# Kernel optimization log

Hardware: AMD Instinct MI355X
Metric: run time of the kernel (lower is better)

The kernel has to match this reference:

```python
import jax, jax.numpy as jnp
import numpy as np

B, S, D, H = 2, 4096, 768, 12
DK = D // H


def setup_inputs() -> dict:
    key = jax.random.key(0)
    ks = jax.random.split(key, 12)
    inp = {
        "q": jax.random.normal(ks[0], (B, S, D), dtype=jnp.float32),
        "k": jax.random.normal(ks[1], (B, S, D), dtype=jnp.float32),
        "v": jax.random.normal(ks[2], (B, S, D), dtype=jnp.float32),
        "mask": jax.random.randint(ks[3], (B, 1, 1, S), 0, 2, dtype=jnp.int32),
        "w_q": jax.random.normal(ks[4], (D, D), dtype=jnp.float32) * 0.02,
        "b_q": jnp.zeros((D,), dtype=jnp.float32),
        "w_k": jax.random.normal(ks[5], (D, D), dtype=jnp.float32) * 0.02,
        "b_k": jnp.zeros((D,), dtype=jnp.float32),
        "w_v": jax.random.normal(ks[6], (D, D), dtype=jnp.float32) * 0.02,
        "b_v": jnp.zeros((D,), dtype=jnp.float32),
        "w_o": jax.random.normal(ks[7], (D, D), dtype=jnp.float32) * 0.02,
        "b_o": jnp.zeros((D,), dtype=jnp.float32),
    }
    return inp


def reference(q, k, v, mask, w_q, b_q, w_k, b_k, w_v, b_v, w_o, b_o):
    scale = 1.0 / jnp.sqrt(jnp.asarray(DK, dtype=q.dtype))
    # projections, then split heads: [B, S, H, DK]
    Q = (q @ w_q + b_q).reshape(B, S, H, DK)
    K = (k @ w_k + b_k).reshape(B, S, H, DK)
    V = (v @ w_v + b_v).reshape(B, S, H, DK)
    # scores: [B, H, Sq, Sk]
    scores = jnp.einsum("bqhd,bkhd->bhqk", Q, K) * scale
    scores = jnp.where(mask == 0, jnp.asarray(-1e9, dtype=scores.dtype), scores)
    attn = jax.nn.softmax(scores, axis=-1)
    # dropout prob is 0.0 (eval): identity
    out = jnp.einsum("bhqk,bkhd->bqhd", attn, V).reshape(B, S, D)
    return out @ w_o + b_o
```

## Files before the change

### kernel.cpp

```cpp
#include <hip/hip_runtime.h>
#include <hip/hip_bf16.h>
#include <stdint.h>

typedef __bf16 bf16;
typedef bf16 bf16x8 __attribute__((ext_vector_type(8)));
typedef float f32x4 __attribute__((ext_vector_type(4)));

constexpr int CB  = 2;
constexpr int CS  = 4096;
constexpr int CD  = 768;
constexpr int CH  = 12;
constexpr int CDK = 64;
constexpr int CBH = CB * CH;
constexpr int CM  = CB * CS;

__device__ __forceinline__ void gload16(const void* g, void* l) {
  __builtin_amdgcn_global_load_lds((const __attribute__((address_space(1))) void*)g,
                                   (__attribute__((address_space(3))) void*)l, 16, 0, 0);
}

__device__ __forceinline__ float fast_exp2(float x) {
#if __has_builtin(__builtin_amdgcn_exp2f)
  return __builtin_amdgcn_exp2f(x);
#else
  return exp2f(x);
#endif
}

__device__ __forceinline__ uint32_t cvtpk_bf16(float lo, float hi) {
  uint32_t r;
  asm("v_cvt_pk_bf16_f32 %0, %1, %2" : "=v"(r) : "v"(lo), "v"(hi));
  return r;
}

__global__ __launch_bounds__(256) void k_convert(const float* __restrict__ in,
                                                 bf16* __restrict__ out, int n8) {
  int i = blockIdx.x * 256 + threadIdx.x;
  if (i >= n8) return;
  const float4* p = (const float4*)in;
  float4 a = p[i * 2], b = p[i * 2 + 1];
  bf16x8 o;
  o[0] = (bf16)a.x; o[1] = (bf16)a.y; o[2] = (bf16)a.z; o[3] = (bf16)a.w;
  o[4] = (bf16)b.x; o[5] = (bf16)b.y; o[6] = (bf16)b.z; o[7] = (bf16)b.w;
  ((bf16x8*)out)[i] = o;
}

__global__ __launch_bounds__(256) void k_wtrans(const float* __restrict__ w0, const float* __restrict__ w1,
                                                const float* __restrict__ w2, const float* __restrict__ w3,
                                                bf16* __restrict__ o0, bf16* __restrict__ o1,
                                                bf16* __restrict__ o2, bf16* __restrict__ o3) {
  const float* w; bf16* o;
  if      (blockIdx.z == 0) { w = w0; o = o0; }
  else if (blockIdx.z == 1) { w = w1; o = o1; }
  else if (blockIdx.z == 2) { w = w2; o = o2; }
  else                      { w = w3; o = o3; }
  __shared__ float t[32][33];
  int k0 = blockIdx.x * 32, n0 = blockIdx.y * 32;
  int tx = threadIdx.x & 31, ty = threadIdx.x >> 5;
#pragma unroll
  for (int i = 0; i < 4; ++i) {
    int kk = ty + i * 8;
    t[kk][tx] = w[(size_t)(k0 + kk) * CD + n0 + tx];
  }
  __syncthreads();
#pragma unroll
  for (int i = 0; i < 4; ++i) {
    int nn = ty + i * 8;
    o[(size_t)(n0 + nn) * CD + k0 + tx] = (bf16)t[tx][nn];
  }
}

template <int EPI>
__device__ __forceinline__ void gemm_core(const bf16* __restrict__ A, const bf16* __restrict__ Bt,
                                          const float* __restrict__ bias, void* __restrict__ outp,
                                          int K, int mtile, int ntile) {
  __shared__ bf16 As[2][128 * 32];
  __shared__ bf16 Bs[2][128 * 32];
  const int tid = threadIdx.x;
  const int lane = tid & 63;
  const int wid = tid >> 6;
  const int wr = wid >> 1, wc = wid & 1;
  const int r = lane & 15, g = lane >> 4;
  const int m0 = mtile * 128, n0 = ntile * 128;

  f32x4 acc[4][4] = {};

  auto stageAB = [&](int bsel, int kt) {
#pragma unroll
    for (int i = 0; i < 2; ++i) {
      int flat = tid * 8 + i * 2048;
      int rr = flat >> 5, cc = flat & 31;
      gload16(A + (size_t)(m0 + rr) * K + kt + cc, (char*)&As[bsel][0] + (size_t)flat * 2);
    }
#pragma unroll
    for (int i = 0; i < 2; ++i) {
      int flat = tid * 8 + i * 2048;
      int rr = flat >> 5, cc = flat & 31;
      gload16(Bt + (size_t)(n0 + rr) * K + kt + cc, (char*)&Bs[bsel][0] + (size_t)flat * 2);
    }
  };

  stageAB(0, 0);
  const int NKT = K / 32;
  for (int t = 0; t < NKT; ++t) {
    __syncthreads();
    if (t + 1 < NKT) stageAB((t + 1) & 1, (t + 1) * 32);
    const bf16* Asb = &As[t & 1][0];
    const bf16* Bsb = &Bs[t & 1][0];

    bf16x8 af[4], bfr[4];
#pragma unroll
    for (int mi = 0; mi < 4; ++mi)
      af[mi] = *(const bf16x8*)(Asb + (wr * 64 + mi * 16 + r) * 32 + g * 8);
#pragma unroll
    for (int ni = 0; ni < 4; ++ni)
      bfr[ni] = *(const bf16x8*)(Bsb + (wc * 64 + ni * 16 + r) * 32 + g * 8);
#pragma unroll
    for (int mi = 0; mi < 4; ++mi)
#pragma unroll
      for (int ni = 0; ni < 4; ++ni)
        acc[mi][ni] = __builtin_amdgcn_mfma_f32_16x16x32_bf16(af[mi], bfr[ni], acc[mi][ni], 0, 0, 0);
  }

  if (EPI == 0) {
    bf16* o = (bf16*)outp;
#pragma unroll
    for (int ni = 0; ni < 4; ++ni) {
      int col = n0 + wc * 64 + ni * 16 + r;
      float bv = bias[col];
      int h = col >> 6, dk = col & 63;
#pragma unroll
      for (int mi = 0; mi < 4; ++mi) {
#pragma unroll
        for (int q = 0; q < 4; ++q) {
          int row = m0 + wr * 64 + mi * 16 + g * 4 + q;
          int b = row >> 12, s = row & 4095;
          o[(size_t)((b * CH + h) * CS + s) * CDK + dk] = (bf16)(acc[mi][ni][q] + bv);
        }
      }
    }
  } else {
    float* o = (float*)outp;
#pragma unroll
    for (int ni = 0; ni < 4; ++ni) {
      int col = n0 + wc * 64 + ni * 16 + r;
      float bv = bias[col];
#pragma unroll
      for (int mi = 0; mi < 4; ++mi) {
#pragma unroll
        for (int q = 0; q < 4; ++q) {
          int row = m0 + wr * 64 + mi * 16 + g * 4 + q;
          o[(size_t)row * CD + col] = acc[mi][ni][q] + bv;
        }
      }
    }
  }
}

__global__ __launch_bounds__(256) void k_qkv(const bf16* __restrict__ qb, const bf16* __restrict__ kb,
                                             const bf16* __restrict__ vb,
                                             const bf16* __restrict__ wqT, const bf16* __restrict__ wkT,
                                             const bf16* __restrict__ wvT,
                                             const float* __restrict__ bq, const float* __restrict__ bk,
                                             const float* __restrict__ bv,
                                             bf16* __restrict__ Qh, bf16* __restrict__ Kh,
                                             bf16* __restrict__ Vh) {
  const bf16* A; const bf16* W; const float* bias; bf16* O;
  if      (blockIdx.z == 0) { A = qb; W = wqT; bias = bq; O = Qh; }
  else if (blockIdx.z == 1) { A = kb; W = wkT; bias = bk; O = Kh; }
  else                      { A = vb; W = wvT; bias = bv; O = Vh; }
  gemm_core<0>(A, W, bias, O, CD, blockIdx.x, blockIdx.y);
}

__global__ __launch_bounds__(256) void k_out(const bf16* __restrict__ ao, const bf16* __restrict__ woT,
                                             const float* __restrict__ bo, float* __restrict__ out) {
  gemm_core<1>(ao, woT, bo, out, CD, blockIdx.x, blockIdx.y);
}

__global__ __launch_bounds__(256) void k_scan(const int* __restrict__ mask, int* __restrict__ idx,
                                              int* __restrict__ nk) {
  int b = blockIdx.x;
  const int* m = mask + b * CS;
  int tid = threadIdx.x, lane = tid & 63, wv = tid >> 6;
  int base = tid * 16;
  int mv[16];
  const int4* m4 = (const int4*)(m + base);
#pragma unroll
  for (int i = 0; i < 4; ++i) {
    int4 x = m4[i];
    mv[i * 4 + 0] = x.x; mv[i * 4 + 1] = x.y; mv[i * 4 + 2] = x.z; mv[i * 4 + 3] = x.w;
  }
  int local = 0;
#pragma unroll
  for (int j = 0; j < 16; ++j) local += (mv[j] != 0);
  int pre = local;
#pragma unroll
  for (int d = 1; d < 64; d <<= 1) {
    int t = __shfl_up(pre, d, 64);
    if (lane >= d) pre += t;
  }
  __shared__ int wsum[4];
  if (lane == 63) wsum[wv] = pre;
  __syncthreads();
  int woff = 0;
  for (int w = 0; w < wv; ++w) woff += wsum[w];
  int pos = woff + pre - local;
  int* ib = idx + b * CS;
#pragma unroll
  for (int j = 0; j < 16; ++j)
    if (mv[j]) ib[pos++] = base + j;
  if (tid == 255) nk[b] = woff + pre;
}

__global__ __launch_bounds__(256) void k_gather(const bf16* __restrict__ Kh, const bf16* __restrict__ Vh,
                                                const int* __restrict__ idx, const int* __restrict__ nk,
                                                bf16* __restrict__ Kc, bf16* __restrict__ VTc) {
  int bh = blockIdx.y, b = bh / CH;
  int nkb = nk[b];
  int nkp = (nkb + 63) & ~63;
  int i0 = blockIdx.x * 64;
  if (i0 >= nkp) return;
  const int* ib = idx + b * CS;
  int tid = threadIdx.x;
  __shared__ bf16 t[64][72];
#pragma unroll
  for (int i = 0; i < 2; ++i) {
    int f = tid + i * 256;
    int ii = f >> 3, c8 = (f & 7) << 3;
    int gi = i0 + ii;
    bf16x8 kv = {}, vv = {};
    if (gi < nkb) {
      int s = ib[gi];
      kv = *(const bf16x8*)&Kh[((size_t)bh * CS + s) * CDK + c8];
      vv = *(const bf16x8*)&Vh[((size_t)bh * CS + s) * CDK + c8];
    }
    *(bf16x8*)&Kc[((size_t)bh * CS + gi) * CDK + c8] = kv;
#pragma unroll
    for (int j = 0; j < 8; ++j) t[ii][c8 + j] = vv[j];
  }
  __syncthreads();
#pragma unroll
  for (int i = 0; i < 2; ++i) {
    int f = tid + i * 256;
    int d = f >> 3, s8 = (f & 7) << 3;
    bf16x8 vv;
#pragma unroll
    for (int j = 0; j < 8; ++j) vv[j] = t[s8 + j][d];
    *(bf16x8*)&VTc[((size_t)bh * CDK + d) * CS + i0 + s8] = vv;
  }
}

__global__ __launch_bounds__(256) void k_attn(const bf16* __restrict__ Qh, const bf16* __restrict__ Kc,
                                              const bf16* __restrict__ VTc, const int* __restrict__ nk,
                                              bf16* __restrict__ attn_out) {
  __shared__ bf16 Ks[2][64 * 64];
  __shared__ bf16 VTs[2][64 * 64];
  __shared__ bf16 Pl[4][16 * 64];

  const int tid = threadIdx.x;
  const int lane = tid & 63, wv = tid >> 6;
  const int r = lane & 15, g = lane >> 4;
  const int bh = blockIdx.y;
  const int b = bh / CH, h = bh % CH;
  const int q0 = blockIdx.x * 128 + wv * 32;
  const int nkb = nk[b];
  const int ntiles = (nkb + 63) >> 6;

  bf16x8 aq[2][2];
#pragma unroll
  for (int rg = 0; rg < 2; ++rg) {
    size_t qrow = (size_t)bh * CS + q0 + rg * 16 + r;
    aq[rg][0] = *(const bf16x8*)&Qh[qrow * CDK + g * 8];
    aq[rg][1] = *(const bf16x8*)&Qh[qrow * CDK + 32 + g * 8];
  }

  f32x4 accO[2][4] = {};
  float m_run[2] = {0.f, 0.f}, l_run[2] = {0.f, 0.f};

  const float cs = 0.18033688f;
  char* PlB = (char*)&Pl[wv][0];

  auto stage = [&](int bsel, int kt) {
    char* KsB0 = (char*)&Ks[bsel][0];
    char* VTsB0 = (char*)&VTs[bsel][0];
#pragma unroll
    for (int i = 0; i < 2; ++i) {
      int f = tid + i * 256;
      int row = f >> 3, sl = f & 7;
      int srcb = (sl * 16) ^ ((row & 7) << 4);
      gload16(Kc + (size_t)(bh * CS + kt + row) * CDK + (srcb >> 1), KsB0 + (size_t)f * 16);
    }
#pragma unroll
    for (int i = 0; i < 2; ++i) {
      int f = tid + i * 256;
      int row = f >> 3, sl = f & 7;
      int srcb = (sl * 16) ^ ((row & 7) << 4);
      gload16(VTc + (size_t)(bh * CDK + row) * CS + kt + (srcb >> 1), VTsB0 + (size_t)f * 16);
    }
  };

  stage(0, 0);

  for (int t = 0; t < ntiles; ++t) {
    __syncthreads();
    if (t + 1 < ntiles) stage((t + 1) & 1, (t + 1) * 64);
    const int kt = t * 64;
    char* KsB = (char*)&Ks[t & 1][0];
    char* VTsB = (char*)&VTs[t & 1][0];
    const bool tail = (kt + 64 > nkb);

#pragma unroll
    for (int rg = 0; rg < 2; ++rg) {
      float p[16];
#pragma unroll
      for (int kb = 0; kb < 4; ++kb) {
        f32x4 s = {};
#pragma unroll
        for (int kh = 0; kh < 2; ++kh) {
          int key = kb * 16 + r;
          int byteoff = key * 128 + ((kh * 64 + g * 16) ^ ((key & 7) << 4));
          bf16x8 ka = *(const bf16x8*)(KsB + byteoff);
          s = __builtin_amdgcn_mfma_f32_16x16x32_bf16(ka, aq[rg][kh], s, 0, 0, 0);
        }
#pragma unroll
        for (int q = 0; q < 4; ++q) p[kb * 4 + q] = s[q] * cs;
      }
      if (tail) {
#pragma unroll
        for (int kb = 0; kb < 4; ++kb)
#pragma unroll
          for (int q = 0; q < 4; ++q)
            if (kt + kb * 16 + g * 4 + q >= nkb) p[kb * 4 + q] = -1e30f;
      }

      float pm = p[0];
#pragma unroll
      for (int j = 1; j < 16; ++j) pm = fmaxf(pm, p[j]);
      pm = fmaxf(pm, __shfl_xor(pm, 16, 64));
      pm = fmaxf(pm, __shfl_xor(pm, 32, 64));

      if (__any(pm > m_run[rg] + 8.f)) {
        float mnew = fmaxf(m_run[rg], pm);
        float corr = fast_exp2(m_run[rg] - mnew);
        m_run[rg] = mnew;
        l_run[rg] *= corr;
#pragma unroll
        for (int q = 0; q < 4; ++q) {
          float cq = __shfl(corr, 20 * g + q, 64);
#pragma unroll
          for (int nb = 0; nb < 4; ++nb) accO[rg][nb][q] *= cq;
        }
      }

      float rsum = 0.f;
#pragma unroll
      for (int kb = 0; kb < 4; ++kb) {
        float e0 = fast_exp2(p[kb * 4 + 0] - m_run[rg]);
        float e1 = fast_exp2(p[kb * 4 + 1] - m_run[rg]);
        float e2 = fast_exp2(p[kb * 4 + 2] - m_run[rg]);
        float e3 = fast_exp2(p[kb * 4 + 3] - m_run[rg]);
        rsum += (e0 + e1) + (e2 + e3);
        uint2 w;
        w.x = cvtpk_bf16(e0, e1);
        w.y = cvtpk_bf16(e2, e3);
        int byteoff = r * 128 + ((kb * 32 + g * 8) ^ ((r & 7) << 4));
        *(uint2*)(PlB + byteoff) = w;
      }
      rsum += __shfl_xor(rsum, 16, 64);
      rsum += __shfl_xor(rsum, 32, 64);
      l_run[rg] += rsum;

      bf16x8 pa[2];
#pragma unroll
      for (int kh = 0; kh < 2; ++kh) {
        int byteoff = r * 128 + ((kh * 64 + g * 16) ^ ((r & 7) << 4));
        pa[kh] = *(const bf16x8*)(PlB + byteoff);
      }
#pragma unroll
      for (int nb = 0; nb < 4; ++nb) {
#pragma unroll
        for (int kh = 0; kh < 2; ++kh) {
          int d = nb * 16 + r;
          int byteoff = d * 128 + ((kh * 64 + g * 16) ^ ((d & 7) << 4));
          bf16x8 bvf = *(const bf16x8*)(VTsB + byteoff);
          accO[rg][nb] = __builtin_amdgcn_mfma_f32_16x16x32_bf16(pa[kh], bvf, accO[rg][nb], 0, 0, 0);
        }
      }
    }
  }

#pragma unroll
  for (int rg = 0; rg < 2; ++rg) {
#pragma unroll
    for (int q = 0; q < 4; ++q) {
      float lq = __shfl(l_run[rg], 20 * g + q, 64);
      float inv = 1.f / lq;
      int srow = q0 + rg * 16 + g * 4 + q;
      size_t bs = (size_t)b * CS + srow;
#pragma unroll
      for (int nb = 0; nb < 4; ++nb) {
        int d = nb * 16 + r;
        attn_out[bs * CD + h * 64 + d] = (bf16)(accO[rg][nb][q] * inv);
      }
    }
  }
}

extern "C" void kernel_launch(void* const* d_in, const int* in_sizes, int n_in,
                              void* d_out, int out_size, void* d_ws, size_t ws_size,
                              hipStream_t stream) {
  const float* q   = (const float*)d_in[0];
  const float* k   = (const float*)d_in[1];
  const float* v   = (const float*)d_in[2];
  const int*  mask = (const int*)d_in[3];
  const float* w_q = (const float*)d_in[4];
  const float* b_q = (const float*)d_in[5];
  const float* w_k = (const float*)d_in[6];
  const float* b_k = (const float*)d_in[7];
  const float* w_v = (const float*)d_in[8];
  const float* b_v = (const float*)d_in[9];
  const float* w_o = (const float*)d_in[10];
  const float* b_o = (const float*)d_in[11];

  char* ws = (char*)d_ws;
  size_t off = 0;
  auto alloc = [&](size_t bytes) { char* p = ws + off; off += (bytes + 255) & ~255ULL; return p; };

  const size_t MD2 = (size_t)CM * CD * 2;
  const size_t WT2 = (size_t)CD * CD * 2;
  bf16* qb  = (bf16*)alloc(MD2);
  bf16* kb  = (bf16*)alloc(MD2);
  bf16* vb  = (bf16*)alloc(MD2);
  bf16* wqT = (bf16*)alloc(WT2);
  bf16* wkT = (bf16*)alloc(WT2);
  bf16* wvT = (bf16*)alloc(WT2);
  bf16* woT = (bf16*)alloc(WT2);
  bf16* Qh  = (bf16*)alloc(MD2);
  bf16* Kh  = (bf16*)alloc(MD2);
  bf16* Vh  = (bf16*)alloc(MD2);
  int*  idx = (int*)alloc((size_t)CB * CS * 4);
  int*  nkd = (int*)alloc(256);
  bf16* Kc  = qb;
  bf16* VTc = kb;
  bf16* ao  = vb;
  (void)ws_size; (void)in_sizes; (void)n_in; (void)out_size;

  const int n8 = CM * CD / 8;
  dim3 blk(256);

  k_convert<<<dim3((n8 + 255) / 256), blk, 0, stream>>>(q, qb, n8);
  k_convert<<<dim3((n8 + 255) / 256), blk, 0, stream>>>(k, kb, n8);
  k_convert<<<dim3((n8 + 255) / 256), blk, 0, stream>>>(v, vb, n8);
  k_wtrans<<<dim3(CD / 32, CD / 32, 4), blk, 0, stream>>>(w_q, w_k, w_v, w_o, wqT, wkT, wvT, woT);
  k_scan<<<dim3(CB), blk, 0, stream>>>(mask, idx, nkd);
  k_qkv<<<dim3(CM / 128, CD / 128, 3), blk, 0, stream>>>(qb, kb, vb, wqT, wkT, wvT, b_q, b_k, b_v, Qh, Kh, Vh);
  k_gather<<<dim3(CS / 64, CBH), blk, 0, stream>>>(Kh, Vh, idx, nkd, Kc, VTc);
  k_attn<<<dim3(CS / 128, CBH), blk, 0, stream>>>(Qh, Kc, VTc, nkd, ao);
  k_out<<<dim3(CM / 128, CD / 128), blk, 0, stream>>>(ao, woT, b_o, (float*)d_out);
}
```

Measured before the change: 191.0 us.

## Keep attention probabilities in registers, merge convert launches, add MFMA priority hints

The attention kernel now permutes which key each lane's score row covers. The probability fragment produced by QK^T can then feed the PV MFMA directly from registers, removing the per-wave LDS round trip for P. The K swizzle and tail mask are adjusted to match the new key mapping. Separately, the three fp32-to-bf16 conversions become a single launch, and s_setprio hints wrap the MFMA blocks in the GEMM and attention loops. The permuted layout risks correctness or bank conflicts if the mapping is subtly wrong.

```diff
diff --git a/kernel.cpp b/kernel.cpp
--- a/kernel.cpp
+++ b/kernel.cpp
@@ -33,8 +33,14 @@
   return r;
 }
 
-__global__ __launch_bounds__(256) void k_convert(const float* __restrict__ in,
-                                                 bf16* __restrict__ out, int n8) {
+__global__ __launch_bounds__(256) void k_convert3(const float* __restrict__ q, const float* __restrict__ k,
+                                                  const float* __restrict__ v,
+                                                  bf16* __restrict__ qo, bf16* __restrict__ ko,
+                                                  bf16* __restrict__ vo, int n8) {
+  const float* in; bf16* out;
+  if      (blockIdx.y == 0) { in = q; out = qo; }
+  else if (blockIdx.y == 1) { in = k; out = ko; }
+  else                      { in = v; out = vo; }
   int i = blockIdx.x * 256 + threadIdx.x;
   if (i >= n8) return;
   const float4* p = (const float4*)in;
@@ -115,11 +121,13 @@
 #pragma unroll
     for (int ni = 0; ni < 4; ++ni)
       bfr[ni] = *(const bf16x8*)(Bsb + (wc * 64 + ni * 16 + r) * 32 + g * 8);
+    __builtin_amdgcn_s_setprio(1);
 #pragma unroll
     for (int mi = 0; mi < 4; ++mi)
 #pragma unroll
       for (int ni = 0; ni < 4; ++ni)
         acc[mi][ni] = __builtin_amdgcn_mfma_f32_16x16x32_bf16(af[mi], bfr[ni], acc[mi][ni], 0, 0, 0);
+    __builtin_amdgcn_s_setprio(0);
   }
 
   if (EPI == 0) {
@@ -250,12 +258,13 @@
   }
 }
 
+__device__ __forceinline__ int KSWZ(int key) { return ((key & 3) + ((key >> 3) & 1) * 4) << 4; }
+
 __global__ __launch_bounds__(256) void k_attn(const bf16* __restrict__ Qh, const bf16* __restrict__ Kc,
                                               const bf16* __restrict__ VTc, const int* __restrict__ nk,
                                               bf16* __restrict__ attn_out) {
   __shared__ bf16 Ks[2][64 * 64];
   __shared__ bf16 VTs[2][64 * 64];
-  __shared__ bf16 Pl[4][16 * 64];
 
   const int tid = threadIdx.x;
   const int lane = tid & 63, wv = tid >> 6;
@@ -278,7 +287,6 @@
   float m_run[2] = {0.f, 0.f}, l_run[2] = {0.f, 0.f};
 
   const float cs = 0.18033688f;
-  char* PlB = (char*)&Pl[wv][0];
 
   auto stage = [&](int bsel, int kt) {
     char* KsB0 = (char*)&Ks[bsel][0];
@@ -287,7 +295,7 @@
     for (int i = 0; i < 2; ++i) {
       int f = tid + i * 256;
       int row = f >> 3, sl = f & 7;
-      int srcb = (sl * 16) ^ ((row & 7) << 4);
+      int srcb = (sl * 16) ^ KSWZ(row);
       gload16(Kc + (size_t)(bh * CS + kt + row) * CDK + (srcb >> 1), KsB0 + (size_t)f * 16);
     }
 #pragma unroll
@@ -312,25 +320,27 @@
 #pragma unroll
     for (int rg = 0; rg < 2; ++rg) {
       float p[16];
+      __builtin_amdgcn_s_setprio(1);
 #pragma unroll
       for (int kb = 0; kb < 4; ++kb) {
+        const int key = 8 * (r >> 2) + 32 * (kb >> 1) + 4 * (kb & 1) + (r & 3);
         f32x4 s = {};
 #pragma unroll
         for (int kh = 0; kh < 2; ++kh) {
-          int key = kb * 16 + r;
-          int byteoff = key * 128 + ((kh * 64 + g * 16) ^ ((key & 7) << 4));
+          int byteoff = key * 128 + ((kh * 64 + g * 16) ^ KSWZ(key));
           bf16x8 ka = *(const bf16x8*)(KsB + byteoff);
           s = __builtin_amdgcn_mfma_f32_16x16x32_bf16(ka, aq[rg][kh], s, 0, 0, 0);
         }
 #pragma unroll
         for (int q = 0; q < 4; ++q) p[kb * 4 + q] = s[q] * cs;
       }
+      __builtin_amdgcn_s_setprio(0);
       if (tail) {
 #pragma unroll
         for (int kb = 0; kb < 4; ++kb)
 #pragma unroll
           for (int q = 0; q < 4; ++q)
-            if (kt + kb * 16 + g * 4 + q >= nkb) p[kb * 4 + q] = -1e30f;
+            if (kt + 8 * g + 32 * (kb >> 1) + 4 * (kb & 1) + q >= nkb) p[kb * 4 + q] = -1e30f;
       }
 
       float pm = p[0];
@@ -353,6 +363,7 @@
       }
 
       float rsum = 0.f;
+      union { uint32_t u[8]; bf16x8 v[2]; } pk;
 #pragma unroll
       for (int kb = 0; kb < 4; ++kb) {
         float e0 = fast_exp2(p[kb * 4 + 0] - m_run[rg]);
@@ -360,22 +371,14 @@
         float e2 = fast_exp2(p[kb * 4 + 2] - m_run[rg]);
         float e3 = fast_exp2(p[kb * 4 + 3] - m_run[rg]);
         rsum += (e0 + e1) + (e2 + e3);
-        uint2 w;
-        w.x = cvtpk_bf16(e0, e1);
-        w.y = cvtpk_bf16(e2, e3);
-        int byteoff = r * 128 + ((kb * 32 + g * 8) ^ ((r & 7) << 4));
-        *(uint2*)(PlB + byteoff) = w;
+        pk.u[kb * 2 + 0] = cvtpk_bf16(e0, e1);
+        pk.u[kb * 2 + 1] = cvtpk_bf16(e2, e3);
       }
       rsum += __shfl_xor(rsum, 16, 64);
       rsum += __shfl_xor(rsum, 32, 64);
       l_run[rg] += rsum;
 
-      bf16x8 pa[2];
-#pragma unroll
-      for (int kh = 0; kh < 2; ++kh) {
-        int byteoff = r * 128 + ((kh * 64 + g * 16) ^ ((r & 7) << 4));
-        pa[kh] = *(const bf16x8*)(PlB + byteoff);
-      }
+      __builtin_amdgcn_s_setprio(1);
 #pragma unroll
       for (int nb = 0; nb < 4; ++nb) {
 #pragma unroll
@@ -383,9 +386,10 @@
           int d = nb * 16 + r;
           int byteoff = d * 128 + ((kh * 64 + g * 16) ^ ((d & 7) << 4));
           bf16x8 bvf = *(const bf16x8*)(VTsB + byteoff);
-          accO[rg][nb] = __builtin_amdgcn_mfma_f32_16x16x32_bf16(pa[kh], bvf, accO[rg][nb], 0, 0, 0);
+          accO[rg][nb] = __builtin_amdgcn_mfma_f32_16x16x32_bf16(pk.v[kh], bvf, accO[rg][nb], 0, 0, 0);
         }
       }
+      __builtin_amdgcn_s_setprio(0);
     }
   }
 
@@ -448,9 +452,7 @@
   const int n8 = CM * CD / 8;
   dim3 blk(256);
 
-  k_convert<<<dim3((n8 + 255) / 256), blk, 0, stream>>>(q, qb, n8);
-  k_convert<<<dim3((n8 + 255) / 256), blk, 0, stream>>>(k, kb, n8);
-  k_convert<<<dim3((n8 + 255) / 256), blk, 0, stream>>>(v, vb, n8);
+  k_convert3<<<dim3((n8 + 255) / 256, 3), blk, 0, stream>>>(q, k, v, qb, kb, vb, n8);
   k_wtrans<<<dim3(CD / 32, CD / 32, 4), blk, 0, stream>>>(w_q, w_k, w_v, w_o, wqT, wkT, wvT, woT);
   k_scan<<<dim3(CB), blk, 0, stream>>>(mask, idx, nkd);
   k_qkv<<<dim3(CM / 128, CD / 128, 3), blk, 0, stream>>>(qb, kb, vb, wqT, wkT, wvT, b_q, b_k, b_v, Qh, Kh, Vh);
```

Measured after the change: 186.0 us. 1.03x faster.
